# Optimization experiments

Hardware: AMD Instinct MI355X
Metric: run time of the kernel (lower is better)

## Reference

```python
import jax, jax.numpy as jnp
import numpy as np

D_MODEL = 512
N_HEAD = 8
D_HEAD = D_MODEL // N_HEAD


def _linear(x, W, b):
    return x @ W + b


def setup_inputs() -> dict:
    key = jax.random.key(0)
    ks = jax.random.split(key, 20)
    B, N, D = 8, 1024, D_MODEL
    H = D // 2
    s = 1.0 / np.sqrt(D)
    s2 = 1.0 / np.sqrt(H)
    inp = {
        'query': jax.random.normal(ks[0], (B, N, D), jnp.float32),
        'key_in': jax.random.normal(ks[1], (B, N, D), jnp.float32),
        'value': jax.random.normal(ks[2], (B, N, D), jnp.float32),
        'Wq': jax.random.normal(ks[3], (D, D), jnp.float32) * s,
        'bq': jnp.zeros((D,), jnp.float32),
        'Wk': jax.random.normal(ks[4], (D, D), jnp.float32) * s,
        'bk': jnp.zeros((D,), jnp.float32),
        'Wv': jax.random.normal(ks[5], (D, D), jnp.float32) * s,
        'bv': jnp.zeros((D,), jnp.float32),
        'Wo': jax.random.normal(ks[6], (D, D), jnp.float32) * s,
        'bo': jnp.zeros((D,), jnp.float32),
        'Ws1': jax.random.normal(ks[7], (D, H), jnp.float32) * s,
        'bs1': jnp.zeros((H,), jnp.float32),
        'Ws2': jax.random.normal(ks[8], (H, D), jnp.float32) * s2,
        'bs2': jnp.zeros((D,), jnp.float32),
        'Wc1': jax.random.normal(ks[9], (D, H), jnp.float32) * s,
        'bc1': jnp.zeros((H,), jnp.float32),
        'Wc2': jax.random.normal(ks[10], (H, D), jnp.float32) * s2,
        'bc2': jnp.zeros((D,), jnp.float32),
    }
    return inp


def reference(query, key_in, value, Wq, bq, Wk, bk, Wv, bv, Wo, bo,
              Ws1, bs1, Ws2, bs2, Wc1, bc1, Wc2, bc2):
    B, N, D = query.shape
    H, Dh = N_HEAD, D_HEAD

    def split_heads(x):  # [b, n, h*d] -> [b, h, n, d]
        return x.reshape(B, N, H, Dh).transpose(0, 2, 1, 3)

    q = split_heads(_linear(query, Wq, bq))
    k = split_heads(_linear(key_in, Wk, bk))
    vv = _linear(value, Wv, bv)  # [b, n, d] == rearrange(v,'b h n d->b n (h d)')

    # spatial gating: Linear-ReLU-Linear-Sigmoid on w_v(value)
    sw = jax.nn.sigmoid(_linear(jax.nn.relu(_linear(vv, Ws1, bs1)), Ws2, bs2))
    v_spatial = split_heads(vv * sw)

    # channel gating: MLP on mean-over-seq profile, broadcast back to seq
    prof = value.mean(axis=1, keepdims=True)  # [b, 1, d]
    cw = jax.nn.sigmoid(_linear(jax.nn.relu(_linear(prof, Wc1, bc1)), Wc2, bc2))
    v_channel = split_heads(_linear(value * cw, Wv, bv))

    v_dual = v_spatial + v_channel

    scores = jnp.einsum('bhqd,bhkd->bhqk', q, k) / np.sqrt(Dh).astype(np.float32)
    attn = jax.nn.softmax(scores, axis=-1)
    out = jnp.einsum('bhqk,bhkd->bhqd', attn, v_dual)
    out = out.transpose(0, 2, 1, 3).reshape(B, N, D)
    return _linear(out, Wo, bo)  # dropout is identity in eval mode
```

## Files before the change

kernel.cpp:

```cpp
#include <hip/hip_runtime.h>

typedef unsigned short u16t;
typedef __bf16  bf8   __attribute__((ext_vector_type(8)));
typedef float   f32x4 __attribute__((ext_vector_type(4)));
typedef unsigned short us4 __attribute__((ext_vector_type(4)));

#define DEV __device__ __forceinline__

DEV float bf2f(u16t u) { union { unsigned u; float f; } x; x.u = ((unsigned)u) << 16; return x.f; }
DEV u16t  f2bf(float f) {
    union { float f; unsigned u; } x; x.f = f;
    unsigned r = x.u + 0x7FFFu + ((x.u >> 16) & 1u);
    return (u16t)(r >> 16);
}
DEV uint4 pack8(const float* v) {
    uint4 r;
    r.x = (unsigned)f2bf(v[0]) | ((unsigned)f2bf(v[1]) << 16);
    r.y = (unsigned)f2bf(v[2]) | ((unsigned)f2bf(v[3]) << 16);
    r.z = (unsigned)f2bf(v[4]) | ((unsigned)f2bf(v[5]) << 16);
    r.w = (unsigned)f2bf(v[6]) | ((unsigned)f2bf(v[7]) << 16);
    return r;
}
DEV void gll16(const void* g, void* l) {
    __builtin_amdgcn_global_load_lds(
        (const __attribute__((address_space(1))) unsigned*)g,
        (__attribute__((address_space(3))) unsigned*)l, 16, 0, 0);
}

#define DMODEL 512
#define SEQ    1024
#define NBATCH 8

__global__ __launch_bounds__(256) void fill_sentinel(float* out, int n)
{
    int i = blockIdx.x * 256 + threadIdx.x;
    if (i < n) out[i] = 100.f;
}

__global__ __launch_bounds__(256) void cvt3(const float* q, const float* k,
                                            const float* v,
                                            u16t* Qb, u16t* Kb, u16t* Vb)
{
    int y = blockIdx.y;
    const float* s = (y == 0) ? q : (y == 1) ? k : v;
    u16t*        d = (y == 0) ? Qb : (y == 1) ? Kb : Vb;
    size_t i = ((size_t)blockIdx.x * 256 + threadIdx.x) * 8;
    float4 a = *(const float4*)(s + i), b = *(const float4*)(s + i + 4);
    float o[8] = {a.x, a.y, a.z, a.w, b.x, b.y, b.z, b.w};
    *(uint4*)&d[i] = pack8(o);
}

__global__ __launch_bounds__(256) void transpose6(
    const float* s0, const float* s1, const float* s2, const float* s3,
    const float* s4, const float* s5,
    u16t* d0, u16t* d1, u16t* d2, u16t* d3, u16t* d4, u16t* d5)
{
    int z = blockIdx.z;
    const float* S; u16t* D; int R, C;
    switch (z) {
        case 0: S = s0; D = d0; R = 512; C = 512; break;
        case 1: S = s1; D = d1; R = 512; C = 512; break;
        case 2: S = s2; D = d2; R = 512; C = 512; break;
        case 3: S = s3; D = d3; R = 512; C = 512; break;
        case 4: S = s4; D = d4; R = 512; C = 256; break;
        default:S = s5; D = d5; R = 256; C = 512; break;
    }
    int c0 = blockIdx.x * 32, r0 = blockIdx.y * 32;
    if (c0 >= C || r0 >= R) return;
    __shared__ u16t tile[32][33];
    int tx = threadIdx.x & 31, ty = threadIdx.x >> 5;
#pragma unroll
    for (int p = 0; p < 4; ++p) {
        int r = ty + p * 8;
        tile[r][tx] = f2bf(S[(size_t)(r0 + r) * C + c0 + tx]);
    }
    __syncthreads();
#pragma unroll
    for (int p = 0; p < 4; ++p) {
        int r = ty + p * 8;
        D[(size_t)(c0 + r) * R + r0 + tx] = tile[tx][r];
    }
}

__global__ __launch_bounds__(256) void colmean(const u16t* Vi, float* prof)
{
    int b = blockIdx.y, z = blockIdx.z;
    int d = blockIdx.x * 256 + threadIdx.x;
    const u16t* p = Vi + (size_t)b * SEQ * DMODEL + (size_t)z * 64 * DMODEL + d;
    float s = 0.f;
#pragma unroll 8
    for (int n = 0; n < 64; ++n) s += bf2f(p[(size_t)n * DMODEL]);
    atomicAdd(&prof[b * DMODEL + d], s * (1.f / 1024.f));
}

__global__ __launch_bounds__(256) void cmlp(const float* prof,
                                            const float* Wc1, const float* bc1,
                                            const float* Wc2, const float* bc2,
                                            u16t* cw)
{
    int b = blockIdx.x, t = threadIdx.x;
    __shared__ float pf[512];
    __shared__ float hf[256];
    pf[t]       = prof[b * 512 + t];
    pf[t + 256] = prof[b * 512 + t + 256];
    __syncthreads();
    float s = bc1[t];
    for (int k = 0; k < 512; ++k) s += pf[k] * Wc1[(size_t)k * 256 + t];
    hf[t] = fmaxf(s, 0.f);
    __syncthreads();
#pragma unroll
    for (int o = 0; o < 2; ++o) {
        int d = t + o * 256;
        float s2 = bc2[d];
        for (int k = 0; k < 256; ++k) s2 += hf[k] * Wc2[(size_t)k * 512 + d];
        cw[b * 512 + d] = f2bf(1.f / (1.f + __expf(-s2)));
    }
}

__global__ __launch_bounds__(256) void scale_wv(const u16t* WvT, const u16t* cw,
                                                u16t* WvTs)
{
    int b = blockIdx.y;
    int idx = blockIdx.x * 2048 + threadIdx.x * 8;
    int k = idx & 511;
    uint4 wv = *(const uint4*)&WvT[idx];
    uint4 cu = *(const uint4*)&cw[b * 512 + k];
    const u16t* wp = (const u16t*)&wv;
    const u16t* cp = (const u16t*)&cu;
    float o[8];
#pragma unroll
    for (int q = 0; q < 8; ++q) o[q] = bf2f(wp[q]) * bf2f(cp[q]);
    *(uint4*)&WvTs[(size_t)b * 262144 + idx] = pack8(o);
}

template<int MINW, int WR, int WC, int WM, int NT>
__global__ __launch_bounds__(256, MINW) void gemmP(
    const u16t* A0, const u16t* A1, const u16t* A2, const u16t* A3,
    const u16t* W0, const u16t* W1, const u16t* W2, const u16t* W3,
    const float* B0, const float* B1, const float* B2, const float* B3,
    void* C0, void* C1, void* C2, void* C3,
    int N, int K, int mode,
    const u16t* VVp, u16t* VdTp,
    int tmask, int outf32, int wbmask)
{
    constexpr int BM = WR * WM * 16;
    constexpr int BN = WC * NT * 16;
    constexpr int PA = BM / 64;
    constexpr int PB = BN / 64;
    constexpr int LPT = PA + PB;

    int z = blockIdx.z;
    const u16t* A  = (z == 0) ? A0 : (z == 1) ? A1 : (z == 2) ? A2 : A3;
    const u16t* W  = (z == 0) ? W0 : (z == 1) ? W1 : (z == 2) ? W2 : W3;
    const float* Bi = (z == 0) ? B0 : (z == 1) ? B1 : (z == 2) ? B2 : B3;
    void*       C  = (z == 0) ? C0 : (z == 1) ? C1 : (z == 2) ? C2 : C3;

    int tstore = (tmask >> z) & 1;

    int tid = threadIdx.x;
    int w = tid >> 6, lane = tid & 63, quad = lane >> 4, l16 = lane & 15;
    int wr = w / WC, wc = w % WC;
    int m0 = blockIdx.x * BM, n0 = blockIdx.y * BN;
    int bb = m0 >> 10;
    if ((wbmask >> z) & 1) W += (size_t)bb * 262144;

    __shared__ __align__(16) u16t As[3][BM * 32];
    __shared__ __align__(16) u16t Bs[3][BN * 32];

    const u16t* srcA[PA];
#pragma unroll
    for (int p = 0; p < PA; ++p) {
        int ci = p * 256 + tid, r = ci >> 2, g = ci & 3;
        srcA[p] = A + (size_t)(m0 + r) * K + (g ^ (r & 3)) * 8;
    }
    const u16t* srcB[PB];
#pragma unroll
    for (int p = 0; p < PB; ++p) {
        int ci = p * 256 + tid, r = ci >> 2, g = ci & 3;
        srcB[p] = W + (size_t)(n0 + r) * K + (g ^ (r & 3)) * 8;
    }

    f32x4 zero = {0.f, 0.f, 0.f, 0.f};
    f32x4 acc[WM][NT];
#pragma unroll
    for (int mi = 0; mi < WM; ++mi)
#pragma unroll
        for (int ni = 0; ni < NT; ++ni) acc[mi][ni] = zero;

    auto stage = [&](int buf, int k0) {
#pragma unroll
        for (int p = 0; p < PA; ++p)
            gll16(srcA[p] + k0, &As[buf][(size_t)(p * 256 + w * 64) * 8]);
#pragma unroll
        for (int p = 0; p < PB; ++p)
            gll16(srcB[p] + k0, &Bs[buf][(size_t)(p * 256 + w * 64) * 8]);
    };
    auto compute = [&](int buf) {
        int sx = l16 & 3;
        bf8 af[WM], bfr[NT];
#pragma unroll
        for (int mi = 0; mi < WM; ++mi)
            af[mi] = *(const bf8*)&As[buf][(wr * WM * 16 + mi * 16 + l16) * 32 + ((quad ^ sx) * 8)];
#pragma unroll
        for (int ni = 0; ni < NT; ++ni)
            bfr[ni] = *(const bf8*)&Bs[buf][(wc * NT * 16 + ni * 16 + l16) * 32 + ((quad ^ sx) * 8)];
#pragma unroll
        for (int mi = 0; mi < WM; ++mi)
#pragma unroll
            for (int ni = 0; ni < NT; ++ni)
                acc[mi][ni] = __builtin_amdgcn_mfma_f32_16x16x32_bf16(af[mi], bfr[ni], acc[mi][ni], 0, 0, 0);
    };

    int nt = K >> 5;
    stage(0, 0);
    stage(1, 32);
    for (int t = 0; t < nt; ++t) {
        if (t + 1 < nt)
            asm volatile("s_waitcnt vmcnt(%0) lgkmcnt(0)" :: "n"(LPT) : "memory");
        else
            asm volatile("s_waitcnt vmcnt(0) lgkmcnt(0)" ::: "memory");
        __builtin_amdgcn_s_barrier();
        __builtin_amdgcn_sched_barrier(0);
        compute(t % 3);
        if (t + 2 < nt) stage((t + 2) % 3, (t + 2) << 5);
    }

#pragma unroll
    for (int mi = 0; mi < WM; ++mi) {
        int grow0 = m0 + wr * WM * 16 + mi * 16 + quad * 4;
#pragma unroll
        for (int ni = 0; ni < NT; ++ni) {
            int gcol = n0 + wc * NT * 16 + ni * 16 + l16;
            float bias = Bi[gcol];
            if (mode == 2) {
                int h = gcol >> 6, dh = gcol & 63;
                int b_ = grow0 >> 10, n_ = grow0 & 1023;
                size_t tbase = (size_t)((b_ * 8 + h) * 64 + dh) * 1024 + n_;
                us4 vc = *(const us4*)&VdTp[tbase];
                us4 pk;
#pragma unroll
                for (int r = 0; r < 4; ++r) {
                    float s = acc[mi][ni][r] + bias;
                    float sw = 1.f / (1.f + __expf(-s));
                    float vvv = bf2f(VVp[(size_t)(grow0 + r) * DMODEL + gcol]);
                    pk[r] = f2bf(vvv * sw + bf2f(vc[r]));
                }
                *(us4*)&VdTp[tbase] = pk;
            } else if (tstore) {
                int h = gcol >> 6, dh = gcol & 63;
                int b_ = grow0 >> 10, n_ = grow0 & 1023;
                us4 pk;
#pragma unroll
                for (int r = 0; r < 4; ++r) pk[r] = f2bf(acc[mi][ni][r] + bias);
                *(us4*)&((u16t*)C)[(size_t)((b_ * 8 + h) * 64 + dh) * 1024 + n_] = pk;
            } else if (outf32) {
#pragma unroll
                for (int r = 0; r < 4; ++r)
                    ((float*)C)[(size_t)(grow0 + r) * N + gcol] = acc[mi][ni][r] + bias;
            } else {
#pragma unroll
                for (int r = 0; r < 4; ++r) {
                    float v = acc[mi][ni][r] + bias;
                    if (mode == 1) v = fmaxf(v, 0.f);
                    ((u16t*)C)[(size_t)(grow0 + r) * N + gcol] = f2bf(v);
                }
            }
        }
    }
}

__global__ __launch_bounds__(256, 2) void attn(const u16t* Q, const u16t* Km,
                                               const u16t* VdT, u16t* Oa)
{
    __shared__ __align__(16) u16t Qs[128 * 64];
    __shared__ __align__(16) u16t Ks[2][64 * 64];
    __shared__ __align__(16) u16t Vs[2][64 * 64];

    int qt = blockIdx.x, bh = blockIdx.y;
    int b = bh >> 3, h = bh & 7;
    int tid = threadIdx.x;
    int w = tid >> 6, lane = tid & 63, quad = lane >> 4, l16 = lane & 15;
    int l7 = l16 & 7;
    int ht = quad >> 1;
    int sA = ((quad & 1) * 32 + l16) * 4;
    int sB = sA + 64;

    const u16t* Qp = Q   + ((size_t)(b * SEQ + qt * 128)) * DMODEL + h * 64;
    const u16t* Kp = Km  + ((size_t)(b * SEQ)) * DMODEL + h * 64;
    const u16t* Vp = VdT + ((size_t)(b * 8 + h)) * 64 * SEQ;

    auto stageKV = [&](int buf, int kt2) {
#pragma unroll
        for (int p = 0; p < 2; ++p) {
            int ci = p * 256 + tid;
            int r = ci >> 3, g = ci & 7;
            int gs = (g ^ (r & 7)) * 8;
            gll16(&Kp[(size_t)(kt2 * 64 + r) * DMODEL + gs], &Ks[buf][(size_t)(p * 256 + w * 64) * 8]);
            gll16(&Vp[(size_t)r * SEQ + kt2 * 64 + gs],      &Vs[buf][(size_t)(p * 256 + w * 64) * 8]);
        }
    };

#pragma unroll
    for (int p = 0; p < 4; ++p) {
        int ci = p * 256 + tid;
        int r = ci >> 3, g = ci & 7;
        int gs = (g ^ (r & 7)) * 8;
        gll16(&Qp[(size_t)r * DMODEL + gs], &Qs[(size_t)(p * 256 + w * 64) * 8]);
    }
    stageKV(0, 0);

    asm volatile("s_waitcnt vmcnt(4)" ::: "memory");
    __builtin_amdgcn_s_barrier();
    bf8 aq[2][2];
#pragma unroll
    for (int qg = 0; qg < 2; ++qg)
#pragma unroll
        for (int ks = 0; ks < 2; ++ks)
            aq[qg][ks] = *(const bf8*)&Qs[(w * 32 + qg * 16 + l16) * 64 + (((ks * 4 + quad) ^ l7) * 8)];

    f32x4 zero = {0.f, 0.f, 0.f, 0.f};
    f32x4 oacc[2][4];
    float l_run[2] = {0.f, 0.f};
#pragma unroll
    for (int qg = 0; qg < 2; ++qg)
#pragma unroll
        for (int r = 0; r < 4; ++r) oacc[qg][r] = zero;

    for (int kt = 0; kt < 16; ++kt) {
        int buf = kt & 1;
        asm volatile("s_waitcnt vmcnt(0) lgkmcnt(0)" ::: "memory");
        __builtin_amdgcn_s_barrier();
        __builtin_amdgcn_sched_barrier(0);

        if (kt + 1 < 16) stageKV(buf ^ 1, kt + 1);

        bf8 bk[2][4];
#pragma unroll
        for (int ks = 0; ks < 2; ++ks) {
            int sG = ((ks * 4 + quad) ^ l7) * 8;
#pragma unroll
            for (int j = 0; j < 4; ++j)
                bk[ks][j] = *(const bf8*)&Ks[buf][(j * 16 + l16) * 64 + sG];
        }
        f32x4 sacc[2][4];
#pragma unroll
        for (int qg = 0; qg < 2; ++qg)
#pragma unroll
            for (int j = 0; j < 4; ++j) sacc[qg][j] = zero;
#pragma unroll
        for (int qg = 0; qg < 2; ++qg)
#pragma unroll
            for (int ks = 0; ks < 2; ++ks)
#pragma unroll
                for (int j = 0; j < 4; ++j)
                    sacc[qg][j] = __builtin_amdgcn_mfma_f32_16x16x32_bf16(bk[ks][j], aq[qg][ks], sacc[qg][j], 0, 0, 0);

        unsigned pks[2][8];
#pragma unroll
        for (int qg = 0; qg < 2; ++qg) {
            float p[4][4];
            float rsum = 0.f;
#pragma unroll
            for (int j = 0; j < 4; ++j)
#pragma unroll
                for (int r = 0; r < 4; ++r) {
                    float xx = fmaf(sacc[qg][j][r], 0.18033688f, -5.77078016f);
                    float pe;
                    asm("v_exp_f32 %0, %1" : "=v"(pe) : "v"(xx));
                    p[j][r] = pe;
                    rsum += pe;
                }
            rsum += __shfl_xor(rsum, 16);
            rsum += __shfl_xor(rsum, 32);
            l_run[qg] += rsum;
#pragma unroll
            for (int j = 0; j < 4; ++j)
#pragma unroll
                for (int c = 0; c < 2; ++c) {
                    union { __bf16 h[2]; unsigned u; } pk;
                    pk.h[0] = (__bf16)p[j][2 * c];
                    pk.h[1] = (__bf16)p[j][2 * c + 1];
                    pks[qg][2 * j + c] = pk.u;
                }
        }

        bf8 bvf[2][4];
#pragma unroll
        for (int ks = 0; ks < 2; ++ks) {
            int sG = ((ks * 4 + quad) ^ l7) * 8;
#pragma unroll
            for (int j = 0; j < 4; ++j)
                bvf[ks][j] = *(const bf8*)&Vs[buf][(j * 16 + l16) * 64 + sG];
        }
#pragma unroll
        for (int qg = 0; qg < 2; ++qg)
#pragma unroll
            for (int ks = 0; ks < 2; ++ks) {
                int rA[4], rB[4];
#pragma unroll
                for (int c = 0; c < 4; ++c) {
                    rA[c] = __builtin_amdgcn_ds_bpermute(sA, (int)pks[qg][ks * 4 + c]);
                    rB[c] = __builtin_amdgcn_ds_bpermute(sB, (int)pks[qg][ks * 4 + c]);
                }
                union { int d[4]; bf8 v; } apu;
                apu.d[0] = ht ? rA[2] : rA[0];
                apu.d[1] = ht ? rA[3] : rA[1];
                apu.d[2] = ht ? rB[2] : rB[0];
                apu.d[3] = ht ? rB[3] : rB[1];
#pragma unroll
                for (int j = 0; j < 4; ++j)
                    oacc[qg][j] = __builtin_amdgcn_mfma_f32_16x16x32_bf16(apu.v, bvf[ks][j], oacc[qg][j], 0, 0, 0);
            }
    }

#pragma unroll
    for (int qg = 0; qg < 2; ++qg) {
        float lr[4];
#pragma unroll
        for (int r4 = 0; r4 < 4; ++r4)
            lr[r4] = __shfl(l_run[qg], (quad << 4) | (quad * 4 + r4));
#pragma unroll
        for (int j = 0; j < 4; ++j) {
#pragma unroll
            for (int r4 = 0; r4 < 4; ++r4) {
                int rq = qt * 128 + w * 32 + qg * 16 + quad * 4 + r4;
                float v = oacc[qg][j][r4] / lr[r4];
                Oa[((size_t)(b * SEQ + rq)) * DMODEL + h * 64 + j * 16 + l16] = f2bf(v);
            }
        }
    }
}

extern "C" void kernel_launch(void* const* d_in, const int* in_sizes, int n_in,
                              void* d_out, int out_size, void* d_ws, size_t ws_size,
                              hipStream_t stream)
{
    const float* query  = (const float*)d_in[0];
    const float* key_in = (const float*)d_in[1];
    const float* value  = (const float*)d_in[2];
    const float* Wq  = (const float*)d_in[3];  const float* bq  = (const float*)d_in[4];
    const float* Wk  = (const float*)d_in[5];  const float* bk  = (const float*)d_in[6];
    const float* Wv  = (const float*)d_in[7];  const float* bv  = (const float*)d_in[8];
    const float* Wo  = (const float*)d_in[9];  const float* bo  = (const float*)d_in[10];
    const float* Ws1 = (const float*)d_in[11]; const float* bs1 = (const float*)d_in[12];
    const float* Ws2 = (const float*)d_in[13]; const float* bs2 = (const float*)d_in[14];
    const float* Wc1 = (const float*)d_in[15]; const float* bc1 = (const float*)d_in[16];
    const float* Wc2 = (const float*)d_in[17]; const float* bc2 = (const float*)d_in[18];
    float* out = (float*)d_out;

    u16t* ws = (u16t*)d_ws;
    u16t* WqT  = ws + 0;
    u16t* WkT  = ws + 262144;
    u16t* WvT  = ws + 524288;
    u16t* WoT  = ws + 786432;
    u16t* Ws1T = ws + 1048576;
    u16t* Ws2T = ws + 1179648;
    u16t* WvTs = ws + 1310720;
    u16t* Vi   = ws + 3407872;
    u16t* Qm   = ws + 7602176;
    u16t* Kmm  = ws + 11796480;
    u16t* VV   = ws + 15990784;
    u16t* VdT  = ws + 20185088;
    u16t* cw   = ws + 24379392;
    float* prof = (float*)(ws + 24383488);
    u16t* Qbf  = ws + 24391680;
    u16t* Kbf  = ws + 28585984;
    u16t* H1 = Vi;
    u16t* Oa = VV;

    const size_t NEED_BYTES = 32780288ull * 2ull;
    if (ws_size < NEED_BYTES) {
        fill_sentinel<<<(out_size + 255) / 256, 256, 0, stream>>>(out, out_size);
        return;
    }

    hipMemsetAsync((void*)prof, 0, NBATCH * DMODEL * sizeof(float), stream);

    cvt3<<<dim3(2048, 3), 256, 0, stream>>>(query, key_in, value, Qbf, Kbf, Vi);
    transpose6<<<dim3(16, 16, 6), 256, 0, stream>>>(Wq, Wk, Wv, Wo, Ws1, Ws2,
                                                    WqT, WkT, WvT, WoT, Ws1T, Ws2T);
    colmean<<<dim3(2, 8, 16), 256, 0, stream>>>(Vi, prof);
    cmlp<<<8, 256, 0, stream>>>(prof, Wc1, bc1, Wc2, bc2, cw);
    scale_wv<<<dim3(128, 8), 256, 0, stream>>>(WvT, cw, WvTs);

    gemmP<2, 2, 2, 4, 8><<<dim3(64, 2, 4), 256, 0, stream>>>(
        Qbf, Kbf, Vi, Vi,
        WqT, WkT, WvT, WvTs,
        bq, bk, bv, bv,
        Qm, Kmm, VV, VdT,
        512, 512, 0, nullptr, VdT,
        0x8, 0, 0x8);

    gemmP<4, 2, 2, 2, 2><<<dim3(128, 4, 1), 256, 0, stream>>>(
        VV, VV, VV, VV, Ws1T, Ws1T, Ws1T, Ws1T, bs1, bs1, bs1, bs1,
        H1, H1, H1, H1, 256, 512, 1, nullptr, nullptr, 0, 0, 0);

    gemmP<4, 2, 2, 2, 2><<<dim3(128, 8, 1), 256, 0, stream>>>(
        H1, H1, H1, H1, Ws2T, Ws2T, Ws2T, Ws2T, bs2, bs2, bs2, bs2,
        Qm, Qm, Qm, Qm,
        512, 256, 2, VV, VdT, 0, 0, 0);

    attn<<<dim3(8, 64), 256, 0, stream>>>(Qm, Kmm, VdT, Oa);

    gemmP<4, 2, 2, 2, 2><<<dim3(128, 8, 1), 256, 0, stream>>>(
        Oa, Oa, Oa, Oa, WoT, WoT, WoT, WoT, bo, bo, bo, bo,
        out, out, out, out, 512, 512, 0, nullptr, nullptr,
        0, 1, 0);
}
```

Before: 262.3 us.

## Stage 128-key tiles per barrier in attention and reorder grid dims

The attention kernel now stages K and V in 128-key tiles, halving the number of barrier/wait iterations from 16 to 8. Each iteration processes two 64-key halves from the same buffer, and the V tile uses a wider XOR swizzle over 16 groups. The grid is also transposed so consecutive blocks share the same (batch, head) K/V, which may improve L2 reuse. In exchange, LDS use grows from about 48KB to 80KB per block, which could limit occupancy.

```diff
diff --git a/kernel.cpp b/kernel.cpp
--- a/kernel.cpp
+++ b/kernel.cpp
@@ -273,10 +273,10 @@
                                                const u16t* VdT, u16t* Oa)
 {
     __shared__ __align__(16) u16t Qs[128 * 64];
-    __shared__ __align__(16) u16t Ks[2][64 * 64];
-    __shared__ __align__(16) u16t Vs[2][64 * 64];
-
-    int qt = blockIdx.x, bh = blockIdx.y;
+    __shared__ __align__(16) u16t Ks[2][128 * 64];
+    __shared__ __align__(16) u16t Vs[2][64 * 128];
+
+    int bh = blockIdx.x, qt = blockIdx.y;
     int b = bh >> 3, h = bh & 7;
     int tid = threadIdx.x;
     int w = tid >> 6, lane = tid & 63, quad = lane >> 4, l16 = lane & 15;
@@ -289,14 +289,16 @@
     const u16t* Kp = Km  + ((size_t)(b * SEQ)) * DMODEL + h * 64;
     const u16t* Vp = VdT + ((size_t)(b * 8 + h)) * 64 * SEQ;
 
-    auto stageKV = [&](int buf, int kt2) {
-#pragma unroll
-        for (int p = 0; p < 2; ++p) {
+    auto stageKV = [&](int buf, int it) {
+#pragma unroll
+        for (int p = 0; p < 4; ++p) {
             int ci = p * 256 + tid;
-            int r = ci >> 3, g = ci & 7;
-            int gs = (g ^ (r & 7)) * 8;
-            gll16(&Kp[(size_t)(kt2 * 64 + r) * DMODEL + gs], &Ks[buf][(size_t)(p * 256 + w * 64) * 8]);
-            gll16(&Vp[(size_t)r * SEQ + kt2 * 64 + gs],      &Vs[buf][(size_t)(p * 256 + w * 64) * 8]);
+            int rk = ci >> 3, gk = ci & 7;
+            gll16(&Kp[(size_t)(it * 128 + rk) * DMODEL + ((gk ^ (rk & 7)) * 8)],
+                  &Ks[buf][(size_t)(p * 256 + w * 64) * 8]);
+            int rv = ci >> 4, gv = ci & 15;
+            gll16(&Vp[(size_t)rv * SEQ + it * 128 + ((gv ^ (rv & 15)) * 8)],
+                  &Vs[buf][(size_t)(p * 256 + w * 64) * 8]);
         }
     };
 
@@ -309,7 +311,7 @@
     }
     stageKV(0, 0);
 
-    asm volatile("s_waitcnt vmcnt(4)" ::: "memory");
+    asm volatile("s_waitcnt vmcnt(8)" ::: "memory");
     __builtin_amdgcn_s_barrier();
     bf8 aq[2][2];
 #pragma unroll
@@ -326,91 +328,96 @@
 #pragma unroll
         for (int r = 0; r < 4; ++r) oacc[qg][r] = zero;
 
-    for (int kt = 0; kt < 16; ++kt) {
-        int buf = kt & 1;
+    for (int it = 0; it < 8; ++it) {
+        int buf = it & 1;
         asm volatile("s_waitcnt vmcnt(0) lgkmcnt(0)" ::: "memory");
         __builtin_amdgcn_s_barrier();
         __builtin_amdgcn_sched_barrier(0);
 
-        if (kt + 1 < 16) stageKV(buf ^ 1, kt + 1);
-
-        bf8 bk[2][4];
-#pragma unroll
-        for (int ks = 0; ks < 2; ++ks) {
-            int sG = ((ks * 4 + quad) ^ l7) * 8;
-#pragma unroll
-            for (int j = 0; j < 4; ++j)
-                bk[ks][j] = *(const bf8*)&Ks[buf][(j * 16 + l16) * 64 + sG];
-        }
-        f32x4 sacc[2][4];
-#pragma unroll
-        for (int qg = 0; qg < 2; ++qg)
-#pragma unroll
-            for (int j = 0; j < 4; ++j) sacc[qg][j] = zero;
-#pragma unroll
-        for (int qg = 0; qg < 2; ++qg)
-#pragma unroll
-            for (int ks = 0; ks < 2; ++ks)
+        if (it + 1 < 8) stageKV(buf ^ 1, it + 1);
+
+#pragma unroll
+        for (int kh = 0; kh < 2; ++kh) {
+            bf8 bk[2][4];
+#pragma unroll
+            for (int ks = 0; ks < 2; ++ks) {
+                int sG = ((ks * 4 + quad) ^ l7) * 8;
 #pragma unroll
                 for (int j = 0; j < 4; ++j)
-                    sacc[qg][j] = __builtin_amdgcn_mfma_f32_16x16x32_bf16(bk[ks][j], aq[qg][ks], sacc[qg][j], 0, 0, 0);
-
-        unsigned pks[2][8];
-#pragma unroll
-        for (int qg = 0; qg < 2; ++qg) {
-            float p[4][4];
-            float rsum = 0.f;
-#pragma unroll
-            for (int j = 0; j < 4; ++j)
-#pragma unroll
-                for (int r = 0; r < 4; ++r) {
-                    float xx = fmaf(sacc[qg][j][r], 0.18033688f, -5.77078016f);
-                    float pe;
-                    asm("v_exp_f32 %0, %1" : "=v"(pe) : "v"(xx));
-                    p[j][r] = pe;
-                    rsum += pe;
+                    bk[ks][j] = *(const bf8*)&Ks[buf][(kh * 64 + j * 16 + l16) * 64 + sG];
+            }
+            f32x4 sacc[2][4];
+#pragma unroll
+            for (int qg = 0; qg < 2; ++qg)
+#pragma unroll
+                for (int j = 0; j < 4; ++j) sacc[qg][j] = zero;
+#pragma unroll
+            for (int qg = 0; qg < 2; ++qg)
+#pragma unroll
+                for (int ks = 0; ks < 2; ++ks)
+#pragma unroll
+                    for (int j = 0; j < 4; ++j)
+                        sacc[qg][j] = __builtin_amdgcn_mfma_f32_16x16x32_bf16(bk[ks][j], aq[qg][ks], sacc[qg][j], 0, 0, 0);
+
+            unsigned pks[2][8];
+#pragma unroll
+            for (int qg = 0; qg < 2; ++qg) {
+                float p[4][4];
+                float rsum = 0.f;
+#pragma unroll
+                for (int j = 0; j < 4; ++j)
+#pragma unroll
+                    for (int r = 0; r < 4; ++r) {
+                        float xx = fmaf(sacc[qg][j][r], 0.18033688f, -5.77078016f);
+                        float pe;
+                        asm("v_exp_f32 %0, %1" : "=v"(pe) : "v"(xx));
+                        p[j][r] = pe;
+                        rsum += pe;
+                    }
+                rsum += __shfl_xor(rsum, 16);
+                rsum += __shfl_xor(rsum, 32);
+                l_run[qg] += rsum;
+#pragma unroll
+                for (int j = 0; j < 4; ++j)
+#pragma unroll
+                    for (int c = 0; c < 2; ++c) {
+                        union { __bf16 hh[2]; unsigned u; } pk;
+                        pk.hh[0] = (__bf16)p[j][2 * c];
+                        pk.hh[1] = (__bf16)p[j][2 * c + 1];
+                        pks[qg][2 * j + c] = pk.u;
+                    }
+            }
+
+            bf8 bvf[2][4];
+#pragma unroll
+            for (int ks = 0; ks < 2; ++ks) {
+#pragma unroll
+                for (int j = 0; j < 4; ++j) {
+                    int rv = j * 16 + l16;
+                    int sG = (((kh * 8 + ks * 4 + quad) ^ (rv & 15)) * 8);
+                    bvf[ks][j] = *(const bf8*)&Vs[buf][rv * 128 + sG];
                 }
-            rsum += __shfl_xor(rsum, 16);
-            rsum += __shfl_xor(rsum, 32);
-            l_run[qg] += rsum;
-#pragma unroll
-            for (int j = 0; j < 4; ++j)
-#pragma unroll
-                for (int c = 0; c < 2; ++c) {
-                    union { __bf16 h[2]; unsigned u; } pk;
-                    pk.h[0] = (__bf16)p[j][2 * c];
-                    pk.h[1] = (__bf16)p[j][2 * c + 1];
-                    pks[qg][2 * j + c] = pk.u;
+            }
+#pragma unroll
+            for (int qg = 0; qg < 2; ++qg)
+#pragma unroll
+                for (int ks = 0; ks < 2; ++ks) {
+                    int rA[4], rB[4];
+#pragma unroll
+                    for (int c = 0; c < 4; ++c) {
+                        rA[c] = __builtin_amdgcn_ds_bpermute(sA, (int)pks[qg][ks * 4 + c]);
+                        rB[c] = __builtin_amdgcn_ds_bpermute(sB, (int)pks[qg][ks * 4 + c]);
+                    }
+                    union { int d[4]; bf8 v; } apu;
+                    apu.d[0] = ht ? rA[2] : rA[0];
+                    apu.d[1] = ht ? rA[3] : rA[1];
+                    apu.d[2] = ht ? rB[2] : rB[0];
+                    apu.d[3] = ht ? rB[3] : rB[1];
+#pragma unroll
+                    for (int j = 0; j < 4; ++j)
+                        oacc[qg][j] = __builtin_amdgcn_mfma_f32_16x16x32_bf16(apu.v, bvf[ks][j], oacc[qg][j], 0, 0, 0);
                 }
         }
-
-        bf8 bvf[2][4];
-#pragma unroll
-        for (int ks = 0; ks < 2; ++ks) {
-            int sG = ((ks * 4 + quad) ^ l7) * 8;
-#pragma unroll
-            for (int j = 0; j < 4; ++j)
-                bvf[ks][j] = *(const bf8*)&Vs[buf][(j * 16 + l16) * 64 + sG];
-        }
-#pragma unroll
-        for (int qg = 0; qg < 2; ++qg)
-#pragma unroll
-            for (int ks = 0; ks < 2; ++ks) {
-                int rA[4], rB[4];
-#pragma unroll
-                for (int c = 0; c < 4; ++c) {
-                    rA[c] = __builtin_amdgcn_ds_bpermute(sA, (int)pks[qg][ks * 4 + c]);
-                    rB[c] = __builtin_amdgcn_ds_bpermute(sB, (int)pks[qg][ks * 4 + c]);
-                }
-                union { int d[4]; bf8 v; } apu;
-                apu.d[0] = ht ? rA[2] : rA[0];
-                apu.d[1] = ht ? rA[3] : rA[1];
-                apu.d[2] = ht ? rB[2] : rB[0];
-                apu.d[3] = ht ? rB[3] : rB[1];
-#pragma unroll
-                for (int j = 0; j < 4; ++j)
-                    oacc[qg][j] = __builtin_amdgcn_mfma_f32_16x16x32_bf16(apu.v, bvf[ks][j], oacc[qg][j], 0, 0, 0);
-            }
     }
 
 #pragma unroll
@@ -500,7 +507,7 @@
         Qm, Qm, Qm, Qm,
         512, 256, 2, VV, VdT, 0, 0, 0);
 
-    attn<<<dim3(8, 64), 256, 0, stream>>>(Qm, Kmm, VdT, Oa);
+    attn<<<dim3(64, 8), 256, 0, stream>>>(Qm, Kmm, VdT, Oa);
 
     gemmP<4, 2, 2, 2, 2><<<dim3(128, 8, 1), 256, 0, stream>>>(
         Oa, Oa, Oa, Oa, WoT, WoT, WoT, WoT, bo, bo, bo, bo,
```

New measurement: 259.8 us, median of 2. No clear change (-1.0%).
